# Optimization experiments

Hardware: AMD Instinct MI355X
Metric: run time of the kernel (lower is better)

The kernel has to match this reference:

```python
import jax, jax.numpy as jnp
import numpy as np
from jax import lax

# ---- constants matching init_kwargs ----
NY, NX = 1024, 1024
DX, DY = 50.0, 50.0
TTOT = 32.0
DTMAX = 0.5
RHO, G, FD = 910.0, 9.81, 1e-17
EPS = 1e-10
T_FREQ = 5.0
N_STEPS = 64            # fixed step count (>= TTOT/DTMAX); dt masked to 0 once time >= TTOT
LAPSE = 0.0065          # degC per m elevation lapse rate (SMB model)
MELT_FACTOR = 0.5       # m ice / (degC * yr) ablation factor (SMB model)


def update_smb(Z_surf, precip, T_ma_lowest, T_mj_lowest, ice_mask):
    # Lapse-rate temperatures at the surface
    T_ma = T_ma_lowest - LAPSE * Z_surf   # mean annual temperature
    T_mj = T_mj_lowest - LAPSE * Z_surf   # mean July temperature
    accumulation = precip * (T_ma < 0.0).astype(Z_surf.dtype)
    ablation = MELT_FACTOR * jnp.maximum(T_mj, 0.0)
    return (accumulation - ablation) * ice_mask


def setup_inputs() -> dict:
    key = jax.random.key(0)
    k1, k2, k3 = jax.random.split(key, 3)
    # smooth mountain topography: 2500 m gaussian massif + small noise
    y = np.arange(NY, dtype=np.float32) * DY
    x = np.arange(NX, dtype=np.float32) * DX
    yy, xx = np.meshgrid(y, x, indexing="ij")
    cy, cx = y.mean(), x.mean()
    sigma = 0.25 * NX * DX
    z = 2500.0 * np.exp(-((yy - cy) ** 2 + (xx - cx) ** 2) / (2.0 * sigma ** 2))
    Z_topo = jnp.asarray(z, dtype=jnp.float32) + 5.0 * jax.random.normal(k1, (NY, NX), dtype=jnp.float32)
    precip_tensor = 2.0 * jax.random.uniform(k2, (NY, NX), dtype=jnp.float32)  # m ice / yr
    T_ma_lowest = jnp.float32(8.0) + jax.random.normal(k3, (), dtype=jnp.float32)
    T_mj_lowest = T_ma_lowest + jnp.float32(8.0)
    ice_mask = jnp.ones((NY, NX), dtype=jnp.float32)
    return {"precip_tensor": precip_tensor, "T_ma_lowest": T_ma_lowest,
            "T_mj_lowest": T_mj_lowest, "Z_topo": Z_topo, "ice_mask": ice_mask}


def _glacier_step(carry, _, Z_topo, precip, T_ma_lowest, T_mj_lowest, ice_mask):
    H_ice, Z_surf, smb, time, t_last = carry
    # staggered-grid averages and slopes (SIA diffusion)
    H_avg = 0.25 * (H_ice[:-1, :-1] + H_ice[1:, 1:] + H_ice[:-1, 1:] + H_ice[1:, :-1])
    Sx = (Z_surf[:, 1:] - Z_surf[:, :-1]) / DX
    Sy = (Z_surf[1:, :] - Z_surf[:-1, :]) / DY
    Sx = 0.5 * (Sx[:-1, :] + Sx[1:, :])          # (NY-1, NX-1)
    Sy = 0.5 * (Sy[:, :-1] + Sy[:, 1:])          # (NY-1, NX-1)
    Snorm = jnp.sqrt(Sx ** 2 + Sy ** 2 + EPS)
    D = FD * (RHO * G) ** 3 * H_avg ** 5 * Snorm ** 2 + EPS
    # adaptive CFL dt; torch uses .item() so dt is a non-differentiable constant
    dt = jnp.minimum(min(DX, DY) ** 2 / (2.7 * jnp.max(D)), DTMAX)
    dt = lax.stop_gradient(dt)
    dt = jnp.where(time < TTOT, dt, 0.0)         # freeze once ttot is reached
    qx = -(0.5 * (D[:-1, :] + D[1:, :])) * (Z_surf[1:-1, 1:] - Z_surf[1:-1, :-1]) / DX
    qy = -(0.5 * (D[:, :-1] + D[:, 1:])) * (Z_surf[1:, 1:-1] - Z_surf[:-1, 1:-1]) / DY
    dHdt = -(jnp.diff(qx, axis=1) / DX + jnp.diff(qy, axis=0) / DY)  # (NY-2, NX-2)
    H_new = H_ice.at[1:-1, 1:-1].add(dt * (dHdt + smb[1:-1, 1:-1]))
    H_new = jnp.maximum(H_new, 0.0)
    Z_new = Z_topo + H_new
    time = time + dt
    # refresh SMB every T_FREQ model years
    do_upd = (time - t_last) >= T_FREQ
    smb_new = update_smb(Z_new, precip, T_ma_lowest, T_mj_lowest, ice_mask)
    smb = jnp.where(do_upd, smb_new, smb)
    t_last = jnp.where(do_upd, time, t_last)
    return (H_new, Z_new, smb, time, t_last), None


def reference(precip_tensor, T_ma_lowest, T_mj_lowest, Z_topo, ice_mask):
    H_ice = jnp.zeros((NY, NX), dtype=jnp.float32)
    Z_surf = Z_topo + H_ice
    smb = update_smb(Z_surf, precip_tensor, T_ma_lowest, T_mj_lowest, ice_mask)
    time = jnp.float32(0.0)
    t_last = jnp.float32(0.0)
    step = lambda c, x: _glacier_step(c, x, Z_topo, precip_tensor, T_ma_lowest, T_mj_lowest, ice_mask)
    (H_ice, _, _, _, _), _ = lax.scan(step, (H_ice, Z_surf, smb, time, t_last), None, length=N_STEPS)
    return H_ice
```

## Files before the change

kernel.cpp:

```cpp
#include <hip/hip_runtime.h>
#include <math.h>

#define NYg 1024
#define NXg 1024
#define W   1024
#define NSTEPS 64
#define GRID_N (NYg * W)

#define SLOT_STRIDE 32
#define SLOT_GROUP  256
#define NSLOTG      (NSTEPS + 1)
#define WS_CNT  (NSLOTG * SLOT_GROUP)
#define WS_NBF  (WS_CNT + 8 * 32)
#define WS_CTRL_END (WS_NBF + 256 * 32)
#define WS_GRIDS 32768

constexpr float DXf   = 50.0f;
constexpr float DYf   = 50.0f;
constexpr float TTOTf = 32.0f;
constexpr float DTMAXf= 0.5f;
constexpr float EPSf  = 1e-10f;
constexpr float TFREQ = 5.0f;
constexpr float LAPSE = 0.0065f;
constexpr float MELTF = 0.5f;
constexpr double RHOG = 910.0 * 9.81;
constexpr float  CDf  = (float)(1e-17 * RHOG * RHOG * RHOG);

__device__ __forceinline__ float scloadf(const float* p) {
    return __hip_atomic_load(p, __ATOMIC_RELAXED, __HIP_MEMORY_SCOPE_SYSTEM);
}
__device__ __forceinline__ void scstoref(float* p, float v) {
    __hip_atomic_store(p, v, __ATOMIC_RELAXED, __HIP_MEMORY_SCOPE_SYSTEM);
}
__device__ __forceinline__ unsigned scloadu(const unsigned* p) {
    return __hip_atomic_load(p, __ATOMIC_RELAXED, __HIP_MEMORY_SCOPE_SYSTEM);
}

__device__ __forceinline__ float dfunc(float h00, float h01, float h10, float h11,
                                       float z00, float z01, float z10, float z11)
{
    float havg = 0.25f * (h00 + h11 + h01 + h10);
    float sx = ((z01 - z00) + (z11 - z10)) * (0.5f / DXf);
    float sy = ((z10 - z00) + (z11 - z01)) * (0.5f / DYf);
    float sn = sqrtf(sx * sx + sy * sy + EPSf);
    float h2 = havg * havg;
    float h4 = h2 * h2;
    return CDf * (h4 * havg) * (sn * sn) + EPSf;
}

__global__ __launch_bounds__(256) void k_init(unsigned* __restrict__ ctrl)
{
    int idx = blockIdx.x * blockDim.x + threadIdx.x;
    int stride = gridDim.x * blockDim.x;
    for (int i = idx; i < WS_CTRL_END; i += stride) {
        unsigned v = 0u;
        if (i < SLOT_GROUP && (i & (SLOT_STRIDE - 1)) == 0) v = __float_as_uint(EPSf);
        ctrl[i] = v;
    }
}

__global__ __launch_bounds__(1024, 1) void k_run(
    float* __restrict__ EZ0, float* __restrict__ EZ1,
    float* __restrict__ ED0, float* __restrict__ ED1,
    const float* __restrict__ ztopo, const float* __restrict__ precip,
    const float* __restrict__ mask, const float* __restrict__ tma,
    const float* __restrict__ tmj, unsigned* __restrict__ ctrl,
    float* __restrict__ Hout)
{
    __shared__ float sZ[7][W];
    __shared__ float sHm[5][W];
    __shared__ float sD[6][W];
    __shared__ unsigned su[8];
    __shared__ float smax16[16];

    unsigned* slots = ctrl;
    unsigned* cnt   = ctrl + WS_CNT;
    unsigned* nbf   = ctrl + WS_NBF;

    const int c   = threadIdx.x;
    const int b   = blockIdx.x;
    const int r0  = b * 4;
    const int grp = b & 7;
    const int lane = c & 63, wid = c >> 6;
    const bool hasA = (b > 0), hasB = (b < 255);

    const float TMA = tma[0], TMJ = tmj[0];

    float smbr[5], ztr[5], hN[5];

    #pragma unroll
    for (int q = 0; q < 7; ++q) {
        int r = r0 - 1 + q;
        sZ[q][c] = (r >= 0 && r < NYg) ? ztopo[r * W + c] : 0.0f;
    }
    #pragma unroll
    for (int q = 0; q < 5; ++q) sHm[q][c] = 0.0f;
    #pragma unroll
    for (int q = 0; q < 6; ++q) sD[q][c] = EPSf;
    #pragma unroll
    for (int rr = 0; rr < 5; ++rr) {
        int r = r0 + rr;
        if (r < NYg) {
            float z = ztopo[r * W + c];
            ztr[rr] = z;
            float t_ma = TMA - LAPSE * z;
            float t_mj = TMJ - LAPSE * z;
            float acc  = (t_ma < 0.0f) ? precip[r * W + c] : 0.0f;
            float abl  = MELTF * fmaxf(t_mj, 0.0f);
            smbr[rr] = (acc - abl) * mask[r * W + c];
        } else { ztr[rr] = 0.0f; smbr[rr] = 0.0f; }
    }
    __syncthreads();

    float t = 0.0f, tl = 0.0f;

    for (int s = 0; s < NSTEPS; ++s) {
        const float* EZr = (s & 1) ? EZ1 : EZ0;
        float*       EZw = (s & 1) ? EZ0 : EZ1;
        const float* EDr = (s & 1) ? ED1 : ED0;
        float*       EDw = (s & 1) ? ED0 : ED1;

        if (s > 0) {
            if (c == 0 && hasA)
                while (scloadu(&nbf[(b - 1) * 32]) < (unsigned)s) __builtin_amdgcn_s_sleep(1);
            if (c == 64 && hasB)
                while (scloadu(&nbf[(b + 1) * 32]) < (unsigned)s) __builtin_amdgcn_s_sleep(1);
            __syncthreads();
            if (hasA) { sZ[0][c] = scloadf(EZr + (r0 - 1) * W + c);
                        if (c <= NXg - 2) sD[0][c] = scloadf(EDr + (r0 - 1) * W + c); }
            if (hasB) { sZ[6][c] = scloadf(EZr + (r0 + 5) * W + c);
                        if (c <= NXg - 2) sD[5][c] = scloadf(EDr + (r0 + 4) * W + c); }
            __syncthreads();
        }

        float dh[5], hOld[5], zOld[5];
        bool inter[5];
        #pragma unroll
        for (int rr = 0; rr < 5; ++rr) {
            int r = r0 + rr;
            float zc = 0.0f, hc = 0.0f, d = 0.0f;
            bool iv = false;
            if (r < NYg) {
                zc = sZ[rr + 1][c];
                hc = sHm[rr][c];
                iv = (r >= 1 && r <= NYg - 2 && c >= 1 && c <= NXg - 2);
                if (iv) {
                    float zl = sZ[rr + 1][c - 1], zr = sZ[rr + 1][c + 1];
                    float zt = sZ[rr][c],         zb = sZ[rr + 2][c];
                    float d00 = sD[rr][c - 1],     d01 = sD[rr][c];
                    float d10 = sD[rr + 1][c - 1], d11 = sD[rr + 1][c];
                    float qxR = -0.5f * (d01 + d11) * (zr - zc) * (1.0f / DXf);
                    float qxL = -0.5f * (d00 + d10) * (zc - zl) * (1.0f / DXf);
                    float qyB = -0.5f * (d10 + d11) * (zb - zc) * (1.0f / DYf);
                    float qyT = -0.5f * (d00 + d01) * (zc - zt) * (1.0f / DYf);
                    d = -((qxR - qxL) * (1.0f / DXf) + (qyB - qyT) * (1.0f / DYf));
                }
            }
            dh[rr] = d; hOld[rr] = hc; zOld[rr] = zc; inter[rr] = iv;
        }

        if (c < 8) {
            unsigned tgt = 32u * (unsigned)s;
            while (scloadu(&cnt[c * 32]) < tgt) __builtin_amdgcn_s_sleep(1);
            su[c] = scloadu(&slots[s * SLOT_GROUP + c * SLOT_STRIDE]);
        }
        __syncthreads();

        unsigned mb = su[0];
        #pragma unroll
        for (int q = 1; q < 8; ++q) mb = max(mb, su[q]);
        float mD = __uint_as_float(mb);
        float dt = fminf(2500.0f / (2.7f * mD), DTMAXf);
        if (!(t < TTOTf)) dt = 0.0f;
        float nt  = t + dt;
        bool  upd = (nt - tl) >= TFREQ;

        #pragma unroll
        for (int rr = 0; rr < 5; ++rr) {
            int r = r0 + rr;
            float h, z;
            if (r >= NYg)        { h = 0.0f; z = 0.0f; }
            else if (inter[rr])  { h = fmaxf(hOld[rr] + dt * (dh[rr] + smbr[rr]), 0.0f);
                                   z = ztr[rr] + h; }
            else                 { h = 0.0f; z = zOld[rr]; }
            hN[rr] = h;
            if (r < NYg) {
                sZ[rr + 1][c] = z;
                sHm[rr][c]    = h;
                if (rr == 1 && hasA) scstoref(EZw + r * W + c, z);
                if (rr == 3 && hasB) scstoref(EZw + r * W + c, z);
                if (upd) {
                    float t_ma = TMA - LAPSE * z;
                    float t_mj = TMJ - LAPSE * z;
                    float acc  = (t_ma < 0.0f) ? precip[r * W + c] : 0.0f;
                    float abl  = MELTF * fmaxf(t_mj, 0.0f);
                    smbr[rr] = (acc - abl) * mask[r * W + c];
                }
            }
        }
        __syncthreads();

        if (s < NSTEPS - 1) {
            float m = 0.0f;
            #pragma unroll
            for (int rr = 0; rr < 4; ++rr) {
                int i = r0 + rr;
                if (i <= NYg - 2 && c <= NXg - 2) {
                    float d = dfunc(sHm[rr][c], sHm[rr][c + 1],
                                    sHm[rr + 1][c], sHm[rr + 1][c + 1],
                                    sZ[rr + 1][c], sZ[rr + 1][c + 1],
                                    sZ[rr + 2][c], sZ[rr + 2][c + 1]);
                    sD[rr + 1][c] = d;
                    m = fmaxf(m, d);
                    if (rr == 0 && hasA) scstoref(EDw + i * W + c, d);
                    if (rr == 3 && hasB) scstoref(EDw + i * W + c, d);
                }
            }
            asm volatile("s_waitcnt vmcnt(0)" ::: "memory");
            #pragma unroll
            for (int off = 32; off >= 1; off >>= 1)
                m = fmaxf(m, __shfl_xor(m, off, 64));
            if (lane == 0) smax16[wid] = m;
            __syncthreads();
            if (c == 0) {
                #pragma unroll
                for (int q = 1; q < 16; ++q) m = fmaxf(m, smax16[q]);
                __hip_atomic_fetch_max(&slots[(s + 1) * SLOT_GROUP + grp * SLOT_STRIDE],
                                       __float_as_uint(m),
                                       __ATOMIC_RELAXED, __HIP_MEMORY_SCOPE_SYSTEM);
                asm volatile("s_waitcnt vmcnt(0)" ::: "memory");
                __hip_atomic_fetch_add(&cnt[grp * 32], 1u,
                                       __ATOMIC_RELAXED, __HIP_MEMORY_SCOPE_SYSTEM);
                __hip_atomic_store(&nbf[b * 32], (unsigned)(s + 1),
                                   __ATOMIC_RELAXED, __HIP_MEMORY_SCOPE_SYSTEM);
            }
        }

        t = nt;
        if (upd) tl = nt;
    }

    #pragma unroll
    for (int rr = 0; rr < 4; ++rr)
        Hout[(r0 + rr) * W + c] = hN[rr];
}

extern "C" void kernel_launch(void* const* d_in, const int* in_sizes, int n_in,
                              void* d_out, int out_size, void* d_ws, size_t ws_size,
                              hipStream_t stream)
{
    const float* precip = (const float*)d_in[0];
    const float* tma    = (const float*)d_in[1];
    const float* tmj    = (const float*)d_in[2];
    const float* ztopo  = (const float*)d_in[3];
    const float* mask   = (const float*)d_in[4];

    unsigned* ctrl = (unsigned*)d_ws;
    float* g = (float*)d_ws + WS_GRIDS;
    float* EZ0 = g + 0 * GRID_N;
    float* EZ1 = g + 1 * GRID_N;
    float* ED0 = g + 2 * GRID_N;
    float* ED1 = g + 3 * GRID_N;

    k_init<<<dim3(64), dim3(256), 0, stream>>>(ctrl);

    k_run<<<dim3(256), dim3(1024), 0, stream>>>(EZ0, EZ1, ED0, ED1,
                                                ztopo, precip, mask, tma, tmj,
                                                ctrl, (float*)d_out);
}
```

Measured before the change: 462.0 us.

## Split grid into 512 two-row blocks with 16 reduction groups and polling backoff

Each persistent block now owns 2 rows instead of 4, so 512 blocks run instead of 256, likely two per CU. The per-step max reduction uses 16 slot groups of 32 blocks, and halo exchange collapses to a single shared boundary row per neighbor pair. Spin-wait loops gain an escalating sleep backoff to reduce contention on the flag and counter lines. The goal is more resident waves to hide latency and less redundant work per block. The cost is more blocks taking part in the grid-wide synchronization, and correctness depends on all 512 blocks being co-resident.

Result: slower. 578.8 us (+25.3%).

```diff
diff --git a/kernel.cpp b/kernel.cpp
--- a/kernel.cpp
+++ b/kernel.cpp
@@ -6,14 +6,16 @@
 #define W   1024
 #define NSTEPS 64
 #define GRID_N (NYg * W)
-
+#define NB    512
+
+#define NSLOT 16
 #define SLOT_STRIDE 32
-#define SLOT_GROUP  256
+#define SLOT_GROUP  (NSLOT * SLOT_STRIDE)
 #define NSLOTG      (NSTEPS + 1)
 #define WS_CNT  (NSLOTG * SLOT_GROUP)
-#define WS_NBF  (WS_CNT + 8 * 32)
-#define WS_CTRL_END (WS_NBF + 256 * 32)
-#define WS_GRIDS 32768
+#define WS_NBF  (WS_CNT + NSLOT * 32)
+#define WS_CTRL_END (WS_NBF + NB * 32)
+#define WS_GRIDS 65536
 
 constexpr float DXf   = 50.0f;
 constexpr float DYf   = 50.0f;
@@ -36,6 +38,11 @@
     return __hip_atomic_load(p, __ATOMIC_RELAXED, __HIP_MEMORY_SCOPE_SYSTEM);
 }
 
+__device__ __forceinline__ void poll_backoff(int& sp) {
+    if (sp < 32) { __builtin_amdgcn_s_sleep(1); ++sp; }
+    else           __builtin_amdgcn_s_sleep(8);
+}
+
 __device__ __forceinline__ float dfunc(float h00, float h01, float h10, float h11,
                                        float z00, float z01, float z10, float z11)
 {
@@ -59,7 +66,7 @@
     }
 }
 
-__global__ __launch_bounds__(1024, 1) void k_run(
+__global__ __launch_bounds__(1024, 8) void k_run(
     float* __restrict__ EZ0, float* __restrict__ EZ1,
     float* __restrict__ ED0, float* __restrict__ ED1,
     const float* __restrict__ ztopo, const float* __restrict__ precip,
@@ -67,10 +74,10 @@
     const float* __restrict__ tmj, unsigned* __restrict__ ctrl,
     float* __restrict__ Hout)
 {
-    __shared__ float sZ[7][W];
-    __shared__ float sHm[5][W];
-    __shared__ float sD[6][W];
-    __shared__ unsigned su[8];
+    __shared__ float sZ[5][W];
+    __shared__ float sHm[3][W];
+    __shared__ float sD[4][W];
+    __shared__ unsigned su[NSLOT];
     __shared__ float smax16[16];
 
     unsigned* slots = ctrl;
@@ -79,26 +86,26 @@
 
     const int c   = threadIdx.x;
     const int b   = blockIdx.x;
-    const int r0  = b * 4;
-    const int grp = b & 7;
+    const int r0  = b * 2;
+    const int grp = b & (NSLOT - 1);
     const int lane = c & 63, wid = c >> 6;
-    const bool hasA = (b > 0), hasB = (b < 255);
+    const bool hasA = (b > 0), hasB = (b < NB - 1);
 
     const float TMA = tma[0], TMJ = tmj[0];
 
-    float smbr[5], ztr[5], hN[5];
-
-    #pragma unroll
-    for (int q = 0; q < 7; ++q) {
+    float smbr[3], ztr[3], hN[3];
+
+    #pragma unroll
+    for (int q = 0; q < 5; ++q) {
         int r = r0 - 1 + q;
         sZ[q][c] = (r >= 0 && r < NYg) ? ztopo[r * W + c] : 0.0f;
     }
     #pragma unroll
-    for (int q = 0; q < 5; ++q) sHm[q][c] = 0.0f;
-    #pragma unroll
-    for (int q = 0; q < 6; ++q) sD[q][c] = EPSf;
-    #pragma unroll
-    for (int rr = 0; rr < 5; ++rr) {
+    for (int q = 0; q < 3; ++q) sHm[q][c] = 0.0f;
+    #pragma unroll
+    for (int q = 0; q < 4; ++q) sD[q][c] = EPSf;
+    #pragma unroll
+    for (int rr = 0; rr < 3; ++rr) {
         int r = r0 + rr;
         if (r < NYg) {
             float z = ztopo[r * W + c];
@@ -121,22 +128,26 @@
         float*       EDw = (s & 1) ? ED0 : ED1;
 
         if (s > 0) {
-            if (c == 0 && hasA)
-                while (scloadu(&nbf[(b - 1) * 32]) < (unsigned)s) __builtin_amdgcn_s_sleep(1);
-            if (c == 64 && hasB)
-                while (scloadu(&nbf[(b + 1) * 32]) < (unsigned)s) __builtin_amdgcn_s_sleep(1);
+            if (c == 0 && hasA) {
+                int sp = 0;
+                while (scloadu(&nbf[(b - 1) * 32]) < (unsigned)s) poll_backoff(sp);
+            }
+            if (c == 64 && hasB) {
+                int sp = 0;
+                while (scloadu(&nbf[(b + 1) * 32]) < (unsigned)s) poll_backoff(sp);
+            }
             __syncthreads();
             if (hasA) { sZ[0][c] = scloadf(EZr + (r0 - 1) * W + c);
                         if (c <= NXg - 2) sD[0][c] = scloadf(EDr + (r0 - 1) * W + c); }
-            if (hasB) { sZ[6][c] = scloadf(EZr + (r0 + 5) * W + c);
-                        if (c <= NXg - 2) sD[5][c] = scloadf(EDr + (r0 + 4) * W + c); }
+            if (hasB) { sZ[4][c] = scloadf(EZr + (r0 + 3) * W + c);
+                        if (c <= NXg - 2) sD[3][c] = scloadf(EDr + (r0 + 2) * W + c); }
             __syncthreads();
         }
 
-        float dh[5], hOld[5], zOld[5];
-        bool inter[5];
+        float dh[3], hOld[3], zOld[3];
+        bool inter[3];
         #pragma unroll
-        for (int rr = 0; rr < 5; ++rr) {
+        for (int rr = 0; rr < 3; ++rr) {
             int r = r0 + rr;
             float zc = 0.0f, hc = 0.0f, d = 0.0f;
             bool iv = false;
@@ -159,16 +170,17 @@
             dh[rr] = d; hOld[rr] = hc; zOld[rr] = zc; inter[rr] = iv;
         }
 
-        if (c < 8) {
+        if (c < NSLOT) {
             unsigned tgt = 32u * (unsigned)s;
-            while (scloadu(&cnt[c * 32]) < tgt) __builtin_amdgcn_s_sleep(1);
+            int sp = 0;
+            while (scloadu(&cnt[c * 32]) < tgt) poll_backoff(sp);
             su[c] = scloadu(&slots[s * SLOT_GROUP + c * SLOT_STRIDE]);
         }
         __syncthreads();
 
         unsigned mb = su[0];
         #pragma unroll
-        for (int q = 1; q < 8; ++q) mb = max(mb, su[q]);
+        for (int q = 1; q < NSLOT; ++q) mb = max(mb, su[q]);
         float mD = __uint_as_float(mb);
         float dt = fminf(2500.0f / (2.7f * mD), DTMAXf);
         if (!(t < TTOTf)) dt = 0.0f;
@@ -176,7 +188,7 @@
         bool  upd = (nt - tl) >= TFREQ;
 
         #pragma unroll
-        for (int rr = 0; rr < 5; ++rr) {
+        for (int rr = 0; rr < 3; ++rr) {
             int r = r0 + rr;
             float h, z;
             if (r >= NYg)        { h = 0.0f; z = 0.0f; }
@@ -187,8 +199,7 @@
             if (r < NYg) {
                 sZ[rr + 1][c] = z;
                 sHm[rr][c]    = h;
-                if (rr == 1 && hasA) scstoref(EZw + r * W + c, z);
-                if (rr == 3 && hasB) scstoref(EZw + r * W + c, z);
+                if (rr == 1) scstoref(EZw + r * W + c, z);
                 if (upd) {
                     float t_ma = TMA - LAPSE * z;
                     float t_mj = TMJ - LAPSE * z;
@@ -203,7 +214,7 @@
         if (s < NSTEPS - 1) {
             float m = 0.0f;
             #pragma unroll
-            for (int rr = 0; rr < 4; ++rr) {
+            for (int rr = 0; rr < 2; ++rr) {
                 int i = r0 + rr;
                 if (i <= NYg - 2 && c <= NXg - 2) {
                     float d = dfunc(sHm[rr][c], sHm[rr][c + 1],
@@ -213,7 +224,7 @@
                     sD[rr + 1][c] = d;
                     m = fmaxf(m, d);
                     if (rr == 0 && hasA) scstoref(EDw + i * W + c, d);
-                    if (rr == 3 && hasB) scstoref(EDw + i * W + c, d);
+                    if (rr == 1 && hasB) scstoref(EDw + i * W + c, d);
                 }
             }
             asm volatile("s_waitcnt vmcnt(0)" ::: "memory");
@@ -241,7 +252,7 @@
     }
 
     #pragma unroll
-    for (int rr = 0; rr < 4; ++rr)
+    for (int rr = 0; rr < 2; ++rr)
         Hout[(r0 + rr) * W + c] = hN[rr];
 }
 
@@ -264,7 +275,7 @@
 
     k_init<<<dim3(64), dim3(256), 0, stream>>>(ctrl);
 
-    k_run<<<dim3(256), dim3(1024), 0, stream>>>(EZ0, EZ1, ED0, ED1,
-                                                ztopo, precip, mask, tma, tmj,
-                                                ctrl, (float*)d_out);
-}
+    k_run<<<dim3(NB), dim3(1024), 0, stream>>>(EZ0, EZ1, ED0, ED1,
+                                               ztopo, precip, mask, tma, tmj,
+                                               ctrl, (float*)d_out);
+}
```
